# Kernel optimization log

Hardware: AMD Instinct MI355X
Metric: run time of the kernel (lower is better)

Reference implementation:

```python
import jax, jax.numpy as jnp
import numpy as np

EMBED_DIM = 1024
NUM_HEADS = 16
RANK = 32
HEAD_DIM = EMBED_DIM // NUM_HEADS
SCALE = 1.0 / np.sqrt(RANK).astype(np.float32)


def setup_inputs() -> dict:
    key = jax.random.key(0)
    ks = jax.random.split(key, 9)
    B, S = 2, 2048
    def lin(k, fan_in, fan_out):
        bound = 1.0 / np.sqrt(fan_in)
        return jax.random.uniform(k, (fan_in, fan_out), jnp.float32, -bound, bound)
    return {
        "hidden_states": jax.random.normal(ks[0], (B, S, EMBED_DIM), jnp.float32),
        "Wq": lin(ks[1], EMBED_DIM, RANK * NUM_HEADS),
        "bq": jnp.zeros((RANK * NUM_HEADS,), jnp.float32),
        "Wk": lin(ks[2], EMBED_DIM, RANK * NUM_HEADS),
        "bk": jnp.zeros((RANK * NUM_HEADS,), jnp.float32),
        "Wv": lin(ks[3], EMBED_DIM, EMBED_DIM),
        "bv": jnp.zeros((EMBED_DIM,), jnp.float32),
        "Wo": lin(ks[4], EMBED_DIM, EMBED_DIM),
        "bo": jnp.zeros((EMBED_DIM,), jnp.float32),
    }


def reference(hidden_states, Wq, bq, Wk, bk, Wv, bv, Wo, bo):
    B, S, E = hidden_states.shape
    q = (hidden_states @ Wq + bq).reshape(B, S, NUM_HEADS, RANK)      # [b,i,h,r]
    k = (hidden_states @ Wk + bk).reshape(B, S, NUM_HEADS, RANK)      # [b,j,h,r]
    v = (hidden_states @ Wv + bv).reshape(B, S, NUM_HEADS, HEAD_DIM)  # [b,j,h,d]
    # full [b,i,j,h] score tensor, softmax over j (axis=2), as in the torch code
    scores = jnp.einsum('bihr,bjhr->bijh', q, k) * SCALE
    attn = jax.nn.softmax(scores, axis=2)
    out = jnp.einsum('bijh,bjhd->bihd', attn, v).reshape(B, S, E)
    return out @ Wo + bo
```

## Files before the change

kernel.cpp:

```cpp
#include <hip/hip_runtime.h>

#define EMBED   1024
#define NHEADS  16
#define RANK    32
#define HDIM    64
#define BATCH   2
#define SEQ     2048
#define BSQ     (BATCH * SEQ)
#define CEXP    0.25505998f

typedef __attribute__((ext_vector_type(8))) short bf16x8;
typedef __attribute__((ext_vector_type(4))) float f32x4;

__device__ __forceinline__ float bf2f(unsigned short u) {
    union { unsigned int i; float f; } x; x.i = ((unsigned int)u) << 16;
    return x.f;
}
__device__ __forceinline__ unsigned short f2bf(float f) {
    union { float f; unsigned int i; } x; x.f = f;
    unsigned int r = x.i + 0x7FFFu + ((x.i >> 16) & 1u);
    return (unsigned short)(r >> 16);
}

#define ASYNC16(gp, lp) \
    __builtin_amdgcn_global_load_lds( \
        (const __attribute__((address_space(1))) void*)(gp), \
        (__attribute__((address_space(3))) void*)(lp), 16, 0, 0)

__global__ __launch_bounds__(256) void prep_all(
    const float* __restrict__ hs,
    const float* __restrict__ Wq, const float* __restrict__ Wk,
    const float* __restrict__ Wv, const float* __restrict__ Wo,
    const float* __restrict__ bq, const float* __restrict__ bk,
    const float* __restrict__ bv,
    unsigned short* __restrict__ hsb, unsigned short* __restrict__ wT_all,
    unsigned short* __restrict__ woT, float* __restrict__ ball)
{
    __shared__ float L[64][65];
    const int blk = blockIdx.x;
    const int t = threadIdx.x;

    if (blk < 2048) {
        const size_t i = ((size_t)blk * 256 + t) * 8;
        float4 v0 = *(const float4*)(hs + i);
        float4 v1 = *(const float4*)(hs + i + 4);
        ushort4 o0, o1;
        o0.x = f2bf(v0.x); o0.y = f2bf(v0.y); o0.z = f2bf(v0.z); o0.w = f2bf(v0.w);
        o1.x = f2bf(v1.x); o1.y = f2bf(v1.y); o1.z = f2bf(v1.z); o1.w = f2bf(v1.w);
        *(ushort4*)(hsb + i) = o0;
        *(ushort4*)(hsb + i + 4) = o1;
        return;
    }
    if (blk < 2816) {
        int idx = blk - 2048;
        int z, bx, by;
        if (idx < 256) { z = idx >> 7; int r2 = idx & 127; bx = r2 & 7; by = r2 >> 3; }
        else { idx -= 256; z = 2 + (idx >> 8); int r2 = idx & 255; bx = r2 & 15; by = r2 >> 4; }
        const int Nw = (z < 2) ? 512 : 1024;
        const float* W = (z == 0) ? Wq : (z == 1) ? Wk : (z == 2) ? Wv : Wo;
        unsigned short* dst = (z == 3) ? woT : (wT_all + (size_t)z * 512 * 1024);

        const int r = t >> 2, c0 = (t & 3) * 16;
        const float* src = W + (size_t)(by * 64 + r) * Nw + bx * 64 + c0;
        #pragma unroll
        for (int u = 0; u < 4; u++)
            *(float4*)&L[r][c0 + 4 * u] = *(const float4*)(src + 4 * u);
        __syncthreads();
        unsigned short* drow = dst + (size_t)(bx * 64 + r) * 1024 + by * 64 + c0;
        #pragma unroll
        for (int u4 = 0; u4 < 4; u4++) {
            ushort4 o;
            o.x = f2bf(L[c0 + 4 * u4 + 0][r]);
            o.y = f2bf(L[c0 + 4 * u4 + 1][r]);
            o.z = f2bf(L[c0 + 4 * u4 + 2][r]);
            o.w = f2bf(L[c0 + 4 * u4 + 3][r]);
            *(ushort4*)(drow + 4 * u4) = o;
        }
        return;
    }
    {
        const int i = (blk - 2816) * 256 + t;
        ball[i] = (i < 512) ? bq[i] : (i < 1024) ? bk[i - 512] : bv[i - 1024];
    }
}

__global__ __launch_bounds__(256) void gemm_qkv(
    const unsigned short* __restrict__ A, const unsigned short* __restrict__ BT,
    const float* __restrict__ bias,
    unsigned short* __restrict__ qH, unsigned short* __restrict__ kH,
    unsigned short* __restrict__ vTout)
{
    __shared__ unsigned short As[2 * 128 * 32];
    __shared__ unsigned short Bs[2 * 128 * 32];
    const int K = 1024;
    const int t = threadIdx.x;
    const int lane = t & 63;
    const int li = lane & 15, la = lane >> 4;
    const int w = t >> 6, wm = w >> 1, wn = w & 1;
    const int row0 = blockIdx.y * 128, col0 = blockIdx.x * 128;

    const int sr = lane >> 2, sc2 = (lane & 3) * 8;
    const unsigned short* ag = A + (size_t)(row0 + sr) * K + sc2;
    const unsigned short* bg = BT + (size_t)(col0 + sr) * K + sc2;

    f32x4 acc[4][4];
    #pragma unroll
    for (int i = 0; i < 4; i++)
        #pragma unroll
        for (int j = 0; j < 4; j++)
            acc[i][j] = (f32x4){0.f, 0.f, 0.f, 0.f};

    for (int k0 = 0; k0 < K; k0 += 64) {
        #pragma unroll
        for (int kh = 0; kh < 2; kh++)
            #pragma unroll
            for (int u = 0; u < 2; u++) {
                const int ro = w * 32 + u * 16;
                ASYNC16(ag + (size_t)ro * K + k0 + kh * 32, &As[kh * 4096 + ro * 32]);
                ASYNC16(bg + (size_t)ro * K + k0 + kh * 32, &Bs[kh * 4096 + ro * 32]);
            }
        __syncthreads();
        #pragma unroll
        for (int kh = 0; kh < 2; kh++) {
            bf16x8 af[4], bfr[4];
            #pragma unroll
            for (int mt = 0; mt < 4; mt++)
                af[mt] = *(const bf16x8*)&As[kh * 4096 + (wm * 64 + mt * 16 + li) * 32 + la * 8];
            #pragma unroll
            for (int nt = 0; nt < 4; nt++)
                bfr[nt] = *(const bf16x8*)&Bs[kh * 4096 + (wn * 64 + nt * 16 + li) * 32 + la * 8];
            #pragma unroll
            for (int mt = 0; mt < 4; mt++)
                #pragma unroll
                for (int nt = 0; nt < 4; nt++)
                    acc[mt][nt] = __builtin_amdgcn_mfma_f32_16x16x32_bf16(af[mt], bfr[nt], acc[mt][nt], 0, 0, 0);
        }
        __syncthreads();
    }

    const int bb = row0 >> 11;
    const int jb = (row0 & 2047) + wm * 64;
    #pragma unroll
    for (int nt = 0; nt < 4; nt++) {
        const int col = col0 + wn * 64 + nt * 16 + li;
        const float bval = bias[col];
        if (col < 1024) {
            const int hh = (col & 511) >> 5;
            const int rr = col & 31;
            unsigned short* base = ((col < 512) ? qH : kH)
                + ((size_t)(bb * 16 + hh) * 2048) * 32 + rr;
            #pragma unroll
            for (int mt = 0; mt < 4; mt++)
                #pragma unroll
                for (int r = 0; r < 4; r++)
                    base[(size_t)(jb + mt * 16 + la * 4 + r) * 32] =
                        f2bf(acc[mt][nt][r] + bval);
        } else {
            const int hd = col - 1024;
            unsigned short* dcol = vTout + ((size_t)(bb * 16 + (hd >> 6)) * 64 + (hd & 63)) * SEQ;
            #pragma unroll
            for (int mt = 0; mt < 4; mt++) {
                const int srow = jb + mt * 16 + la * 4;
                ushort4 o;
                o.x = f2bf(acc[mt][nt][0] + bval);
                o.y = f2bf(acc[mt][nt][1] + bval);
                o.z = f2bf(acc[mt][nt][2] + bval);
                o.w = f2bf(acc[mt][nt][3] + bval);
                *(ushort4*)(dcol + srow) = o;
            }
        }
    }
}

__global__ __launch_bounds__(256) void gemm_out(
    const unsigned short* __restrict__ A, const unsigned short* __restrict__ BT,
    const float* __restrict__ bias, float* __restrict__ C)
{
    __shared__ unsigned short As[2 * 64 * 32];
    __shared__ unsigned short Bs[2 * 128 * 32];
    const int K = 1024;
    const int t = threadIdx.x;
    const int lane = t & 63;
    const int li = lane & 15, la = lane >> 4;
    const int w = t >> 6, wm = w >> 1, wn = w & 1;
    const int row0 = blockIdx.y * 64, col0 = blockIdx.x * 128;

    const int sr = lane >> 2, sc2 = (lane & 3) * 8;
    const unsigned short* ag = A + (size_t)(row0 + sr) * K + sc2;
    const unsigned short* bg = BT + (size_t)(col0 + sr) * K + sc2;

    f32x4 acc[2][4];
    #pragma unroll
    for (int i = 0; i < 2; i++)
        #pragma unroll
        for (int j = 0; j < 4; j++)
            acc[i][j] = (f32x4){0.f, 0.f, 0.f, 0.f};

    for (int k0 = 0; k0 < K; k0 += 64) {
        #pragma unroll
        for (int kh = 0; kh < 2; kh++) {
            ASYNC16(ag + (size_t)(w * 16) * K + k0 + kh * 32, &As[kh * 2048 + (w * 16) * 32]);
            #pragma unroll
            for (int u = 0; u < 2; u++) {
                const int ro = w * 32 + u * 16;
                ASYNC16(bg + (size_t)ro * K + k0 + kh * 32, &Bs[kh * 4096 + ro * 32]);
            }
        }
        __syncthreads();
        #pragma unroll
        for (int kh = 0; kh < 2; kh++) {
            bf16x8 af[2], bfr[4];
            #pragma unroll
            for (int mt = 0; mt < 2; mt++)
                af[mt] = *(const bf16x8*)&As[kh * 2048 + (wm * 32 + mt * 16 + li) * 32 + la * 8];
            #pragma unroll
            for (int nt = 0; nt < 4; nt++)
                bfr[nt] = *(const bf16x8*)&Bs[kh * 4096 + (wn * 64 + nt * 16 + li) * 32 + la * 8];
            #pragma unroll
            for (int mt = 0; mt < 2; mt++)
                #pragma unroll
                for (int nt = 0; nt < 4; nt++)
                    acc[mt][nt] = __builtin_amdgcn_mfma_f32_16x16x32_bf16(af[mt], bfr[nt], acc[mt][nt], 0, 0, 0);
        }
        __syncthreads();
    }

    #pragma unroll
    for (int nt = 0; nt < 4; nt++) {
        const int col = col0 + wn * 64 + nt * 16 + li;
        const float bval = bias[col];
        #pragma unroll
        for (int mt = 0; mt < 2; mt++)
            #pragma unroll
            for (int r = 0; r < 4; r++) {
                const int row = row0 + wm * 32 + mt * 16 + la * 4 + r;
                C[(size_t)row * 1024 + col] = acc[mt][nt][r] + bval;
            }
    }
}

__global__ __launch_bounds__(256) void attn_v9(
    const unsigned short* __restrict__ qH,
    const unsigned short* __restrict__ kH,
    const unsigned short* __restrict__ vT,
    unsigned short* __restrict__ ao)
{
    __shared__ unsigned short kt[2][64 * 48];
    __shared__ unsigned short vt[2][64 * 72];
    __shared__ unsigned short P[64 * 72];

    const int t = threadIdx.x;
    const int lane = t & 63;
    const int li = lane & 15, la = lane >> 4;
    const int w = t >> 6;

    const int bh = blockIdx.x & 31;
    const int itile = blockIdx.x >> 5;
    const int i0 = itile * 64;
    const int b = bh >> 4, h = bh & 15;

    bf16x8 qf;
    {
        const unsigned short* qp = qH + ((size_t)bh * 2048 + i0 + w * 16 + li) * 32 + la * 8;
        ushort4 q0 = *(const ushort4*)qp;
        ushort4 q1 = *(const ushort4*)(qp + 4);
        short u[8];
        u[0] = (short)f2bf(bf2f(q0.x) * CEXP);
        u[1] = (short)f2bf(bf2f(q0.y) * CEXP);
        u[2] = (short)f2bf(bf2f(q0.z) * CEXP);
        u[3] = (short)f2bf(bf2f(q0.w) * CEXP);
        u[4] = (short)f2bf(bf2f(q1.x) * CEXP);
        u[5] = (short)f2bf(bf2f(q1.y) * CEXP);
        u[6] = (short)f2bf(bf2f(q1.z) * CEXP);
        u[7] = (short)f2bf(bf2f(q1.w) * CEXP);
        qf = *(const bf16x8*)u;
    }

    bf16x8 vones;
    #pragma unroll
    for (int u2 = 0; u2 < 8; u2++) vones[u2] = (short)0x3F80;

    const int kr = t >> 2, kc = (t & 3) * 8;
    const int vr = t >> 3, vc = (t & 7) * 8;
    const unsigned short* kp = kH + (size_t)bh * 2048 * 32 + (size_t)kr * 32 + kc;
    const unsigned short* vp0 = vT + (size_t)bh * 64 * SEQ + (size_t)vr * SEQ + vc;
    const unsigned short* vp1 = vp0 + (size_t)32 * SEQ;

    f32x4 accO[4], accl;
    accl = (f32x4){0.f, 0.f, 0.f, 0.f};
    #pragma unroll
    for (int dt = 0; dt < 4; dt++) accO[dt] = (f32x4){0.f, 0.f, 0.f, 0.f};
    const int prow = w * 16 + li;

    uint4 kreg  = *(const uint4*)(kp);
    uint4 vreg0 = *(const uint4*)(vp0);
    uint4 vreg1 = *(const uint4*)(vp1);
    *(uint4*)&kt[0][kr * 48 + kc] = kreg;
    *(uint4*)&vt[0][vr * 72 + vc] = vreg0;
    *(uint4*)&vt[0][(vr + 32) * 72 + vc] = vreg1;
    kreg  = *(const uint4*)(kp + 64 * 32);
    vreg0 = *(const uint4*)(vp0 + 64);
    vreg1 = *(const uint4*)(vp1 + 64);

    #define ATTN_BODY(BUF, OTHER, JPRE)                                            \
    {                                                                              \
        __syncthreads();                                                           \
        *(uint4*)&kt[OTHER][kr * 48 + kc] = kreg;                                  \
        *(uint4*)&vt[OTHER][vr * 72 + vc] = vreg0;                                 \
        *(uint4*)&vt[OTHER][(vr + 32) * 72 + vc] = vreg1;                          \
        const int jn = (JPRE) & 2047;                                              \
        kreg  = *(const uint4*)(kp + (size_t)jn * 32);                             \
        vreg0 = *(const uint4*)(vp0 + jn);                                         \
        vreg1 = *(const uint4*)(vp1 + jn);                                         \
        f32x4 sc[4];                                                               \
        _Pragma("unroll")                                                          \
        for (int jt = 0; jt < 4; jt++) {                                           \
            const bf16x8 kf = *(const bf16x8*)&kt[BUF][(jt * 16 + li) * 48 + la * 8]; \
            sc[jt] = __builtin_amdgcn_mfma_f32_16x16x32_bf16(kf, qf, (f32x4){0.f,0.f,0.f,0.f}, 0, 0, 0); \
        }                                                                          \
        _Pragma("unroll")                                                          \
        for (int jt = 0; jt < 4; jt++) {                                           \
            float e0 = __builtin_amdgcn_exp2f(sc[jt][0]);                          \
            float e1 = __builtin_amdgcn_exp2f(sc[jt][1]);                          \
            float e2 = __builtin_amdgcn_exp2f(sc[jt][2]);                          \
            float e3 = __builtin_amdgcn_exp2f(sc[jt][3]);                          \
            uint2 pk;                                                              \
            asm("v_cvt_pk_bf16_f32 %0, %1, %2" : "=v"(pk.x) : "v"(e0), "v"(e1));   \
            asm("v_cvt_pk_bf16_f32 %0, %1, %2" : "=v"(pk.y) : "v"(e2), "v"(e3));   \
            *(uint2*)&P[prow * 72 + jt * 16 + la * 4] = pk;                        \
        }                                                                          \
        _Pragma("unroll")                                                          \
        for (int ks = 0; ks < 2; ks++) {                                           \
            const bf16x8 pf = *(const bf16x8*)&P[prow * 72 + ks * 32 + la * 8];    \
            accl = __builtin_amdgcn_mfma_f32_16x16x32_bf16(pf, vones, accl, 0, 0, 0); \
            _Pragma("unroll")                                                      \
            for (int dt = 0; dt < 4; dt++) {                                       \
                const bf16x8 vf = *(const bf16x8*)&vt[BUF][(dt * 16 + li) * 72 + ks * 32 + la * 8]; \
                accO[dt] = __builtin_amdgcn_mfma_f32_16x16x32_bf16(pf, vf, accO[dt], 0, 0, 0); \
            }                                                                      \
        }                                                                          \
    }

    for (int j0 = 0; j0 < SEQ; j0 += 128) {
        ATTN_BODY(0, 1, j0 + 128)
        ATTN_BODY(1, 0, j0 + 192)
    }
    #undef ATTN_BODY

    float linv[4];
    #pragma unroll
    for (int r = 0; r < 4; r++) linv[r] = 1.f / accl[r];
    #pragma unroll
    for (int dt = 0; dt < 4; dt++)
        #pragma unroll
        for (int r = 0; r < 4; r++) {
            const int row = b * SEQ + i0 + w * 16 + la * 4 + r;
            ao[(size_t)row * 1024 + h * 64 + dt * 16 + li] = f2bf(accO[dt][r] * linv[r]);
        }
}

extern "C" void kernel_launch(void* const* d_in, const int* in_sizes, int n_in,
                              void* d_out, int out_size, void* d_ws, size_t ws_size,
                              hipStream_t stream) {
    const float* hs = (const float*)d_in[0];
    const float* Wq = (const float*)d_in[1];
    const float* bq = (const float*)d_in[2];
    const float* Wk = (const float*)d_in[3];
    const float* bk = (const float*)d_in[4];
    const float* Wv = (const float*)d_in[5];
    const float* bv = (const float*)d_in[6];
    const float* Wo = (const float*)d_in[7];
    const float* bo = (const float*)d_in[8];

    char* p = (char*)d_ws;
    unsigned short* hsb = (unsigned short*)(p);
    unsigned short* wT  = (unsigned short*)(p + 8388608u);
    unsigned short* woT = (unsigned short*)(p + 12582912u);
    float*          ball= (float*)(p + 14680064u);
    unsigned short* qHb = (unsigned short*)(p + 14688256u);
    unsigned short* kHb = (unsigned short*)(p + 18882560u);
    unsigned short* vTb = (unsigned short*)(p + 23076864u);
    unsigned short* ao  = (unsigned short*)(p + 31465472u);

    prep_all<<<dim3(2824), 256, 0, stream>>>(hs, Wq, Wk, Wv, Wo, bq, bk, bv,
                                             hsb, wT, woT, ball);

    gemm_qkv<<<dim3(16, 32), 256, 0, stream>>>(hsb, wT, ball, qHb, kHb, vTb);

    attn_v9<<<dim3(1024), 256, 0, stream>>>(qHb, kHb, vTb, ao);

    gemm_out<<<dim3(8, 64), 256, 0, stream>>>(ao, woT, bo, (float*)d_out);
}
```

Measured before the change: 181.0 us.

## Load K/V tiles into LDS with async global_load_lds and XOR swizzle

The attention kernel now streams K and V tiles straight from global memory into LDS with global_load_lds, replacing the register-staged loads and LDS stores. Unpadded XOR-swizzled layouts are used so the MFMA fragment reads avoid bank conflicts without padding. The prefetch distance shrinks from two tiles to one, and each iteration waits for all outstanding vector memory ops before the barrier. This saves VGPRs and store instructions but exposes more load latency per tile.

New measurement: 176.4 us. -2.5%, faster.

```diff
diff --git a/kernel.cpp b/kernel.cpp
--- a/kernel.cpp
+++ b/kernel.cpp
@@ -26,6 +26,8 @@
     __builtin_amdgcn_global_load_lds( \
         (const __attribute__((address_space(1))) void*)(gp), \
         (__attribute__((address_space(3))) void*)(lp), 16, 0, 0)
+
+#define VMDRAIN() asm volatile("s_waitcnt vmcnt(0)" ::: "memory")
 
 __global__ __launch_bounds__(256) void prep_all(
     const float* __restrict__ hs,
@@ -239,14 +241,14 @@
     }
 }
 
-__global__ __launch_bounds__(256) void attn_v9(
+__global__ __launch_bounds__(256) void attn_v11(
     const unsigned short* __restrict__ qH,
     const unsigned short* __restrict__ kH,
     const unsigned short* __restrict__ vT,
     unsigned short* __restrict__ ao)
 {
-    __shared__ unsigned short kt[2][64 * 48];
-    __shared__ unsigned short vt[2][64 * 72];
+    __shared__ unsigned short kt[2][64 * 32];
+    __shared__ unsigned short vt[2][64 * 64];
     __shared__ unsigned short P[64 * 72];
 
     const int t = threadIdx.x;
@@ -280,11 +282,17 @@
     #pragma unroll
     for (int u2 = 0; u2 < 8; u2++) vones[u2] = (short)0x3F80;
 
-    const int kr = t >> 2, kc = (t & 3) * 8;
-    const int vr = t >> 3, vc = (t & 7) * 8;
-    const unsigned short* kp = kH + (size_t)bh * 2048 * 32 + (size_t)kr * 32 + kc;
-    const unsigned short* vp0 = vT + (size_t)bh * 64 * SEQ + (size_t)vr * SEQ + vc;
-    const unsigned short* vp1 = vp0 + (size_t)32 * SEQ;
+    const int cK8 = ((lane & 3) ^ ((lane >> 3) & 3)) * 8;
+    const unsigned short* kpt = kH + (size_t)bh * 2048 * 32
+                               + (size_t)(w * 16 + (lane >> 2)) * 32 + cK8;
+    const int rV = lane >> 3;
+    const int cV8 = ((lane & 7) ^ rV) * 8;
+    const unsigned short* vpt0 = vT + ((size_t)bh * 64 + w * 16 + rV) * SEQ + cV8;
+    const unsigned short* vpt1 = vpt0 + (size_t)8 * SEQ;
+
+    const int kcol  = (la ^ ((li >> 1) & 3)) * 8;
+    const int vcol0 = ((0 * 4 + la) ^ (li & 7)) * 8;
+    const int vcol1 = ((1 * 4 + la) ^ (li & 7)) * 8;
 
     f32x4 accO[4], accl;
     accl = (f32x4){0.f, 0.f, 0.f, 0.f};
@@ -292,30 +300,22 @@
     for (int dt = 0; dt < 4; dt++) accO[dt] = (f32x4){0.f, 0.f, 0.f, 0.f};
     const int prow = w * 16 + li;
 
-    uint4 kreg  = *(const uint4*)(kp);
-    uint4 vreg0 = *(const uint4*)(vp0);
-    uint4 vreg1 = *(const uint4*)(vp1);
-    *(uint4*)&kt[0][kr * 48 + kc] = kreg;
-    *(uint4*)&vt[0][vr * 72 + vc] = vreg0;
-    *(uint4*)&vt[0][(vr + 32) * 72 + vc] = vreg1;
-    kreg  = *(const uint4*)(kp + 64 * 32);
-    vreg0 = *(const uint4*)(vp0 + 64);
-    vreg1 = *(const uint4*)(vp1 + 64);
+    ASYNC16(kpt,  &kt[0][w * 512]);
+    ASYNC16(vpt0, &vt[0][w * 1024]);
+    ASYNC16(vpt1, &vt[0][w * 1024 + 512]);
 
     #define ATTN_BODY(BUF, OTHER, JPRE)                                            \
     {                                                                              \
+        VMDRAIN();                                                                 \
         __syncthreads();                                                           \
-        *(uint4*)&kt[OTHER][kr * 48 + kc] = kreg;                                  \
-        *(uint4*)&vt[OTHER][vr * 72 + vc] = vreg0;                                 \
-        *(uint4*)&vt[OTHER][(vr + 32) * 72 + vc] = vreg1;                          \
         const int jn = (JPRE) & 2047;                                              \
-        kreg  = *(const uint4*)(kp + (size_t)jn * 32);                             \
-        vreg0 = *(const uint4*)(vp0 + jn);                                         \
-        vreg1 = *(const uint4*)(vp1 + jn);                                         \
+        ASYNC16(kpt + (size_t)jn * 32, &kt[OTHER][w * 512]);                       \
+        ASYNC16(vpt0 + jn, &vt[OTHER][w * 1024]);                                  \
+        ASYNC16(vpt1 + jn, &vt[OTHER][w * 1024 + 512]);                            \
         f32x4 sc[4];                                                               \
         _Pragma("unroll")                                                          \
         for (int jt = 0; jt < 4; jt++) {                                           \
-            const bf16x8 kf = *(const bf16x8*)&kt[BUF][(jt * 16 + li) * 48 + la * 8]; \
+            const bf16x8 kf = *(const bf16x8*)&kt[BUF][(jt * 16 + li) * 32 + kcol]; \
             sc[jt] = __builtin_amdgcn_mfma_f32_16x16x32_bf16(kf, qf, (f32x4){0.f,0.f,0.f,0.f}, 0, 0, 0); \
         }                                                                          \
         _Pragma("unroll")                                                          \
@@ -333,19 +333,23 @@
         for (int ks = 0; ks < 2; ks++) {                                           \
             const bf16x8 pf = *(const bf16x8*)&P[prow * 72 + ks * 32 + la * 8];    \
             accl = __builtin_amdgcn_mfma_f32_16x16x32_bf16(pf, vones, accl, 0, 0, 0); \
+            const int vcol = ks ? vcol1 : vcol0;                                   \
             _Pragma("unroll")                                                      \
             for (int dt = 0; dt < 4; dt++) {                                       \
-                const bf16x8 vf = *(const bf16x8*)&vt[BUF][(dt * 16 + li) * 72 + ks * 32 + la * 8]; \
+                const bf16x8 vf = *(const bf16x8*)&vt[BUF][(dt * 16 + li) * 64 + vcol]; \
                 accO[dt] = __builtin_amdgcn_mfma_f32_16x16x32_bf16(pf, vf, accO[dt], 0, 0, 0); \
             }                                                                      \
         }                                                                          \
     }
 
     for (int j0 = 0; j0 < SEQ; j0 += 128) {
-        ATTN_BODY(0, 1, j0 + 128)
-        ATTN_BODY(1, 0, j0 + 192)
+        ATTN_BODY(0, 1, j0 + 64)
+        ATTN_BODY(1, 0, j0 + 128)
     }
     #undef ATTN_BODY
+
+    VMDRAIN();
+    __syncthreads();
 
     float linv[4];
     #pragma unroll
@@ -387,7 +391,7 @@
 
     gemm_qkv<<<dim3(16, 32), 256, 0, stream>>>(hsb, wT, ball, qHb, kHb, vTb);
 
-    attn_v9<<<dim3(1024), 256, 0, stream>>>(qHb, kHb, vTb, ao);
+    attn_v11<<<dim3(1024), 256, 0, stream>>>(qHb, kHb, vTb, ao);
 
     gemm_out<<<dim3(8, 64), 256, 0, stream>>>(ao, woT, bo, (float*)d_out);
 }
```
